# Kernel optimization log

Measured on AMD Instinct MI355X. Metric: run time of the kernel, lower is better.

## Reference

```python
import jax, jax.numpy as jnp
import numpy as np

B, P, N, C = 8, 4, 512, 768
H = 12
HD = C // H  # 64
SCALE = HD ** -0.5


def setup_inputs() -> dict:
    key = jax.random.key(0)
    k1, k2, k3 = jax.random.split(key, 3)
    x = jax.random.normal(k1, (B, P, N, C), dtype=jnp.float32)
    W_qkv = jax.random.normal(k2, (3 * C, C), dtype=jnp.float32) * (C ** -0.5)
    W_proj = jax.random.normal(k3, (C, C), dtype=jnp.float32) * (C ** -0.5)
    b_proj = jnp.zeros((C,), dtype=jnp.float32)
    return {"x": x, "W_qkv": W_qkv, "W_proj": W_proj, "b_proj": b_proj}


def reference(x, W_qkv, W_proj, b_proj):
    b, p, n, c = x.shape
    # qkv projection (no bias): (B,P,N,3C) -> (B,P,N,3,H,HD)
    qkv = jnp.einsum('bpnc,dc->bpnd', x, W_qkv).reshape(b, p, n, 3, H, HD)
    # -> (3, B, P, H, N, HD)
    qkv = jnp.transpose(qkv, (3, 0, 1, 4, 2, 5))
    q, k, v = qkv[0], qkv[1], qkv[2]
    # scaled dot-product attention per (batch, patch, head)
    attn = jnp.einsum('bphnd,bphmd->bphnm', q * SCALE, k)
    attn = jax.nn.softmax(attn, axis=-1)
    out = jnp.einsum('bphnm,bphmd->bphnd', attn, v)
    # merge heads: (B,P,N,H,HD) -> (B,P,N,C)
    out = jnp.transpose(out, (0, 1, 3, 2, 4)).reshape(b, p, n, c)
    return jnp.einsum('bpnc,dc->bpnd', out, W_proj) + b_proj
```

## Files before the change

### kernel.cpp

```cpp
#include <hip/hip_runtime.h>

typedef _Float16 f16x8 __attribute__((ext_vector_type(8)));
typedef _Float16 f16x4 __attribute__((ext_vector_type(4)));
typedef unsigned short u16x8 __attribute__((ext_vector_type(8)));
typedef unsigned short u16x4 __attribute__((ext_vector_type(4)));
typedef float f32x4 __attribute__((ext_vector_type(4)));

#define GLOAD_LDS16(GP, LP)                                                        \
  __builtin_amdgcn_global_load_lds((const __attribute__((address_space(1))) void*)(GP), \
                                   (__attribute__((address_space(3))) void*)(LP), 16, 0, 0)

__device__ __forceinline__ unsigned int pkh(float a, float b) {
  return __builtin_bit_cast(unsigned int, __builtin_amdgcn_cvt_pkrtz(a, b));
}
__device__ __forceinline__ f16x8 ldfragh(const unsigned short* p) {
  return __builtin_bit_cast(f16x8, *(const u16x8*)p);
}
__device__ __forceinline__ f16x4 ldfragh4(const unsigned short* p) {
  return __builtin_bit_cast(f16x4, *(const u16x4*)p);
}
__device__ __forceinline__ f32x4 mfma32h(f16x8 a, f16x8 b, f32x4 c) {
  return __builtin_amdgcn_mfma_f32_16x16x32_f16(a, b, c, 0, 0, 0);
}
__device__ __forceinline__ f32x4 mfma16h(f16x4 a, f16x4 b, f32x4 c) {
  return __builtin_amdgcn_mfma_f32_16x16x16f16(a, b, c, 0, 0, 0);
}

#define MTOK   16384
#define CDIM   768
#define C3     2304
#define C2     1536
#define NX     12582912
#define NQW    1769472
#define NPW    589824

#define QSCALE_LOG2E 0.1803368801111204f

#define XB_OFF    0ul
#define WQKV_OFF  25165824ul
#define WPROJ_OFF 28704768ul
#define QK_OFF    29884416ul
#define VT_OFF    80216064ul

__global__ __launch_bounds__(256) void convert_kernel(
    const float* __restrict__ x, const float* __restrict__ wqkv,
    const float* __restrict__ wproj, unsigned short* __restrict__ xb,
    unsigned short* __restrict__ wqkvb, unsigned short* __restrict__ wprojb) {
  const int NX4 = NX / 4, NQ4 = NQW / 4, NP4 = NPW / 4;
  const int total = NX4 + NQ4 + NP4;
  for (int i = blockIdx.x * 256 + threadIdx.x; i < total; i += gridDim.x * 256) {
    const float4* src; unsigned short* dst; float scale = 1.f; int j;
    if (i < NX4) { src = (const float4*)x; dst = xb; j = i; }
    else if (i < NX4 + NQ4) {
      j = i - NX4; src = (const float4*)wqkv; dst = wqkvb;
      int d = (j * 4) / CDIM; if (d < CDIM) scale = QSCALE_LOG2E;
    } else { j = i - NX4 - NQ4; src = (const float4*)wproj; dst = wprojb; }
    float4 v = src[j];
    uint2 pk; pk.x = pkh(v.x * scale, v.y * scale); pk.y = pkh(v.z * scale, v.w * scale);
    *(uint2*)(dst + (long)j * 4) = pk;
  }
}

template <int MODE, int NTN>
__global__ __launch_bounds__(512, 2) void gemm256(
    const unsigned short* __restrict__ A, const unsigned short* __restrict__ B,
    unsigned short* __restrict__ out_hf, unsigned short* __restrict__ out_vT,
    float* __restrict__ out_f32, const float* __restrict__ bias) {
  constexpr int K = 768;
  constexpr int NKT = K / 32;
  __shared__ unsigned short As[4][256 * 32];
  __shared__ unsigned short Bs[4][256 * 32];
  const int tid = threadIdx.x;
  const int wave = tid >> 6, lane = tid & 63;
  const int wy = wave >> 2, wx = wave & 3;
  const int l15 = lane & 15, quad = lane >> 4;

  const int gid = blockIdx.x;
  const int bn = (gid >> 3) % NTN;
  const int bm = ((gid >> 3) / NTN) * 8 + (gid & 7);
  const bool swap = (MODE == 2) || (bn < 6);

  f32x4 acc[8][4];
#pragma unroll
  for (int i = 0; i < 8; i++)
#pragma unroll
    for (int j = 0; j < 4; j++) acc[i][j] = f32x4{0.f, 0.f, 0.f, 0.f};

  const unsigned short* Ab = A + (long)bm * 256 * K;
  const unsigned short* Bb = B + (long)bn * 256 * K;

  const int c0 = wave * 128 + lane;
  const int c1 = c0 + 64;
  const int r0 = c0 >> 2, r1 = c1 >> 2;
  const long g0 = (long)r0 * K + (long)(((c0 & 3) ^ ((r0 >> 2) & 3)) * 8);
  const long g1 = (long)r1 * K + (long)(((c1 & 3) ^ ((r1 >> 2) & 3)) * 8);
  const int s0 = c0 * 8, s1 = c1 * 8;

#define STAGE_A(kt) { GLOAD_LDS16(Ab + g0 + (kt) * 32, &As[(kt) & 3][s0]); \
                      GLOAD_LDS16(Ab + g1 + (kt) * 32, &As[(kt) & 3][s1]); }
#define STAGE_B(kt) { GLOAD_LDS16(Bb + g0 + (kt) * 32, &Bs[(kt) & 3][s0]); \
                      GLOAD_LDS16(Bb + g1 + (kt) * 32, &Bs[(kt) & 3][s1]); }

  STAGE_A(0); STAGE_B(0); STAGE_A(1); STAGE_B(1); STAGE_A(2); STAGE_B(2);
  asm volatile("s_waitcnt vmcnt(8)" ::: "memory");
  __builtin_amdgcn_s_barrier();

  const int pho = (quad ^ (l15 >> 2)) * 8;
  const int arow = wy * 128 + l15;
  const int brow = wx * 64 + l15;

  for (int kt = 0; kt < NKT; kt++) {
    const unsigned short* Ac = As[kt & 3];
    const unsigned short* Bc = Bs[kt & 3];
    f16x8 af[4], bf[4];
#pragma unroll
    for (int nt = 0; nt < 4; nt++) bf[nt] = ldfragh(Bc + (brow + nt * 16) * 32 + pho);
#pragma unroll
    for (int mt = 0; mt < 4; mt++) af[mt] = ldfragh(Ac + (arow + mt * 16) * 32 + pho);
    if (kt < NKT - 3) STAGE_A(kt + 3);
    __builtin_amdgcn_s_barrier();
    asm volatile("s_waitcnt lgkmcnt(0)" ::: "memory");
    __builtin_amdgcn_s_setprio(1);
    if (swap) {
#pragma unroll
      for (int mt = 0; mt < 4; mt++)
#pragma unroll
        for (int nt = 0; nt < 4; nt++)
          acc[mt][nt] = mfma32h(bf[nt], af[mt], acc[mt][nt]);
    } else {
#pragma unroll
      for (int mt = 0; mt < 4; mt++)
#pragma unroll
        for (int nt = 0; nt < 4; nt++)
          acc[mt][nt] = mfma32h(af[mt], bf[nt], acc[mt][nt]);
    }
    __builtin_amdgcn_s_setprio(0);
    __builtin_amdgcn_s_barrier();
#pragma unroll
    for (int mt = 0; mt < 4; mt++) af[mt] = ldfragh(Ac + (arow + 64 + mt * 16) * 32 + pho);
    if (kt < NKT - 3) STAGE_B(kt + 3);
    if (kt < NKT - 3)       { asm volatile("s_waitcnt vmcnt(8)" ::: "memory"); }
    else if (kt == NKT - 3) { asm volatile("s_waitcnt vmcnt(4)" ::: "memory"); }
    else if (kt == NKT - 2) { asm volatile("s_waitcnt vmcnt(0)" ::: "memory"); }
    __builtin_amdgcn_s_barrier();
    asm volatile("s_waitcnt lgkmcnt(0)" ::: "memory");
    __builtin_amdgcn_s_setprio(1);
    if (swap) {
#pragma unroll
      for (int mt = 0; mt < 4; mt++)
#pragma unroll
        for (int nt = 0; nt < 4; nt++)
          acc[4 + mt][nt] = mfma32h(bf[nt], af[mt], acc[4 + mt][nt]);
    } else {
#pragma unroll
      for (int mt = 0; mt < 4; mt++)
#pragma unroll
        for (int nt = 0; nt < 4; nt++)
          acc[4 + mt][nt] = mfma32h(af[mt], bf[nt], acc[4 + mt][nt]);
    }
    __builtin_amdgcn_s_setprio(0);
    __builtin_amdgcn_s_barrier();
  }
#undef STAGE_A
#undef STAGE_B

  if (MODE == 0) {
    if (swap) {
#pragma unroll
      for (int mt = 0; mt < 8; mt++) {
        int m = bm * 256 + wy * 128 + mt * 16 + l15;
#pragma unroll
        for (int nt = 0; nt < 4; nt++) {
          int d0 = bn * 256 + wx * 64 + nt * 16 + quad * 4;
          uint2 pk; pk.x = pkh(acc[mt][nt][0], acc[mt][nt][1]);
          pk.y = pkh(acc[mt][nt][2], acc[mt][nt][3]);
          *(uint2*)(out_hf + (long)m * C2 + d0) = pk;
        }
      }
    } else {
#pragma unroll
      for (int mt = 0; mt < 8; mt++) {
        int mg = bm * 256 + wy * 128 + mt * 16 + quad * 4;
        int bp = mg >> 9, n0 = mg & 511;
#pragma unroll
        for (int nt = 0; nt < 4; nt++) {
          int dp = (bn - 6) * 256 + wx * 64 + nt * 16 + l15;
          int hh = dp >> 6, e = dp & 63;
          uint2 pk; pk.x = pkh(acc[mt][nt][0], acc[mt][nt][1]);
          pk.y = pkh(acc[mt][nt][2], acc[mt][nt][3]);
          *(uint2*)(out_vT + ((long)((bp * 12 + hh) * 64 + e) * 512 + n0)) = pk;
        }
      }
    }
  } else {
#pragma unroll
    for (int nt = 0; nt < 4; nt++) {
      int d0 = bn * 256 + wx * 64 + nt * 16 + quad * 4;
      float4 bv = *(const float4*)(bias + d0);
#pragma unroll
      for (int mt = 0; mt < 8; mt++) {
        int m = bm * 256 + wy * 128 + mt * 16 + l15;
        float4 o;
        o.x = acc[mt][nt][0] + bv.x; o.y = acc[mt][nt][1] + bv.y;
        o.z = acc[mt][nt][2] + bv.z; o.w = acc[mt][nt][3] + bv.w;
        *(float4*)(out_f32 + (long)m * CDIM + d0) = o;
      }
    }
  }
}

__global__ __launch_bounds__(256, 4) void attn_kernel(
    const unsigned short* __restrict__ qk, const unsigned short* __restrict__ vT,
    unsigned short* __restrict__ aout) {
  const int bph = blockIdx.x;
  const int qt  = blockIdx.y;
  const int bp = bph / 12, h = bph % 12;
  const int tid = threadIdx.x;
  const int wave = tid >> 6, lane = tid & 63;
  const int l15 = lane & 15, quad = lane >> 4;

  __shared__ unsigned short Qs[128 * 72];
  __shared__ unsigned short Ks[64 * 72];
  __shared__ unsigned short Vs[64 * 72];

  const unsigned short* Qg = qk + (long)(bp * 512 + qt * 128) * C2 + h * 64;
  const unsigned short* Kg = qk + (long)(bp * 512) * C2 + CDIM + h * 64;
  const unsigned short* Vg = vT + (long)(bp * 12 + h) * 64 * 512;

  for (int i = 0; i < 4; i++) {
    int c = tid + i * 256;
    int row = c >> 3, c8 = c & 7;
    *(uint4*)(Qs + row * 72 + c8 * 8) = *(const uint4*)(Qg + (long)row * C2 + c8 * 8);
  }

  f32x4 o[2][4];
  float lrow[2] = {0.f, 0.f};
  for (int a = 0; a < 2; a++)
    for (int b = 0; b < 4; b++) o[a][b] = f32x4{0.f, 0.f, 0.f, 0.f};

  for (int ch = 0; ch < 8; ch++) {
    if (ch) __syncthreads();
    for (int i = 0; i < 2; i++) {
      int c = tid + i * 256;
      int row = c >> 3, c8 = c & 7;
      *(uint4*)(Ks + row * 72 + c8 * 8) = *(const uint4*)(Kg + (long)(ch * 64 + row) * C2 + c8 * 8);
      *(uint4*)(Vs + row * 72 + c8 * 8) = *(const uint4*)(Vg + (long)row * 512 + ch * 64 + c8 * 8);
    }
    __syncthreads();

    f32x4 st[2][4];
    for (int a = 0; a < 2; a++)
      for (int b = 0; b < 4; b++) st[a][b] = f32x4{0.f, 0.f, 0.f, 0.f};
    for (int ks = 0; ks < 2; ks++) {
      f16x8 qf[2];
      qf[0] = ldfragh(Qs + (wave * 32 +      l15) * 72 + ks * 32 + quad * 8);
      qf[1] = ldfragh(Qs + (wave * 32 + 16 + l15) * 72 + ks * 32 + quad * 8);
      for (int nt = 0; nt < 4; nt++) {
        f16x8 kf = ldfragh(Ks + (nt * 16 + l15) * 72 + ks * 32 + quad * 8);
        st[0][nt] = mfma32h(kf, qf[0], st[0][nt]);
        st[1][nt] = mfma32h(kf, qf[1], st[1][nt]);
      }
    }

    f16x4 pf[2][4];
    for (int mt2 = 0; mt2 < 2; mt2++) {
      float rs = 0.f;
      for (int nt = 0; nt < 4; nt++) {
        f32x4 p;
        for (int r = 0; r < 4; r++) {
          p[r] = __builtin_amdgcn_exp2f(st[mt2][nt][r]);
          rs += p[r];
        }
        uint2 pk2; pk2.x = pkh(p[0], p[1]); pk2.y = pkh(p[2], p[3]);
        pf[mt2][nt] = __builtin_bit_cast(f16x4, pk2);
      }
      lrow[mt2] += rs;
    }

    for (int nt = 0; nt < 4; nt++)
      for (int et = 0; et < 4; et++) {
        f16x4 vf = ldfragh4(Vs + (et * 16 + l15) * 72 + nt * 16 + quad * 4);
        o[0][et] = mfma16h(vf, pf[0][nt], o[0][et]);
        o[1][et] = mfma16h(vf, pf[1][nt], o[1][et]);
      }
  }

  for (int mt2 = 0; mt2 < 2; mt2++) {
    float l = lrow[mt2];
    l += __shfl_xor(l, 16);
    l += __shfl_xor(l, 32);
    float inv = 1.f / l;
    int q = qt * 128 + wave * 32 + mt2 * 16 + l15;
    for (int et = 0; et < 4; et++) {
      uint2 pk; pk.x = pkh(o[mt2][et][0] * inv, o[mt2][et][1] * inv);
      pk.y = pkh(o[mt2][et][2] * inv, o[mt2][et][3] * inv);
      *(uint2*)(aout + (long)(bp * 512 + q) * CDIM + h * 64 + et * 16 + quad * 4) = pk;
    }
  }
}

extern "C" void kernel_launch(void* const* d_in, const int* in_sizes, int n_in,
                              void* d_out, int out_size, void* d_ws, size_t ws_size,
                              hipStream_t stream) {
  (void)in_sizes; (void)n_in; (void)out_size; (void)ws_size;
  const float* x     = (const float*)d_in[0];
  const float* wqkv  = (const float*)d_in[1];
  const float* wproj = (const float*)d_in[2];
  const float* bproj = (const float*)d_in[3];
  float* out = (float*)d_out;
  char* ws = (char*)d_ws;

  unsigned short* xb     = (unsigned short*)(ws + XB_OFF);
  unsigned short* wqkvb  = (unsigned short*)(ws + WQKV_OFF);
  unsigned short* wprojb = (unsigned short*)(ws + WPROJ_OFF);
  unsigned short* qkbuf  = (unsigned short*)(ws + QK_OFF);
  unsigned short* vTbuf  = (unsigned short*)(ws + VT_OFF);
  unsigned short* attn_o = xb;

  convert_kernel<<<2048, 256, 0, stream>>>(x, wqkv, wproj, xb, wqkvb, wprojb);
  gemm256<0, 9><<<576, 512, 0, stream>>>(xb, wqkvb, qkbuf, vTbuf, nullptr, nullptr);
  attn_kernel<<<dim3(384, 4), 256, 0, stream>>>(qkbuf, vTbuf, attn_o);
  gemm256<2, 3><<<192, 512, 0, stream>>>(attn_o, wprojb, nullptr, nullptr, out, bproj);
}
```

Baseline: 290.3 us.

## Retile projection GEMMs to 256x192 tiles with new LDS layout and single barrier per k-step

Changes both GEMMs from 256x256 to 256x192 output tiles, raising the block count (768 and 256) so the 256-CU device gets fuller waves. It replaces the XOR-swizzled LDS staging with a paired-row interleaved layout and merges the two half-k-step phases into one loop body that loads all fragments, then issues 24 MFMAs behind a single barrier. Per-wave vmcnt waits differ because only half the threads stage the extra B chunk. The risks are LDS bank conflicts from the new layout, a WAR hazard on a 4-slot ring now guarded by a single barrier, and more fragment registers in flight.

```diff
diff --git a/kernel.cpp b/kernel.cpp
--- a/kernel.cpp
+++ b/kernel.cpp
@@ -62,14 +62,14 @@
 }
 
 template <int MODE, int NTN>
-__global__ __launch_bounds__(512, 2) void gemm256(
+__global__ __launch_bounds__(512, 2) void gemm192(
     const unsigned short* __restrict__ A, const unsigned short* __restrict__ B,
     unsigned short* __restrict__ out_hf, unsigned short* __restrict__ out_vT,
     float* __restrict__ out_f32, const float* __restrict__ bias) {
   constexpr int K = 768;
-  constexpr int NKT = K / 32;
-  __shared__ unsigned short As[4][256 * 32];
-  __shared__ unsigned short Bs[4][256 * 32];
+  constexpr int NKT = 24;
+  __shared__ unsigned short As[4][8192];
+  __shared__ unsigned short Bs[4][6144];
   const int tid = threadIdx.x;
   const int wave = tid >> 6, lane = tid & 63;
   const int wy = wave >> 2, wx = wave & 3;
@@ -78,91 +78,81 @@
   const int gid = blockIdx.x;
   const int bn = (gid >> 3) % NTN;
   const int bm = ((gid >> 3) / NTN) * 8 + (gid & 7);
-  const bool swap = (MODE == 2) || (bn < 6);
-
-  f32x4 acc[8][4];
+  const bool swap = (MODE == 2) || (bn < 8);
+
+  f32x4 acc[8][3];
 #pragma unroll
   for (int i = 0; i < 8; i++)
 #pragma unroll
-    for (int j = 0; j < 4; j++) acc[i][j] = f32x4{0.f, 0.f, 0.f, 0.f};
+    for (int j = 0; j < 3; j++) acc[i][j] = f32x4{0.f, 0.f, 0.f, 0.f};
 
   const unsigned short* Ab = A + (long)bm * 256 * K;
-  const unsigned short* Bb = B + (long)bn * 256 * K;
-
-  const int c0 = wave * 128 + lane;
-  const int c1 = c0 + 64;
-  const int r0 = c0 >> 2, r1 = c1 >> 2;
-  const long g0 = (long)r0 * K + (long)(((c0 & 3) ^ ((r0 >> 2) & 3)) * 8);
-  const long g1 = (long)r1 * K + (long)(((c1 & 3) ^ ((r1 >> 2) & 3)) * 8);
-  const int s0 = c0 * 8, s1 = c1 * 8;
-
-#define STAGE_A(kt) { GLOAD_LDS16(Ab + g0 + (kt) * 32, &As[(kt) & 3][s0]); \
-                      GLOAD_LDS16(Ab + g1 + (kt) * 32, &As[(kt) & 3][s1]); }
-#define STAGE_B(kt) { GLOAD_LDS16(Bb + g0 + (kt) * 32, &Bs[(kt) & 3][s0]); \
-                      GLOAD_LDS16(Bb + g1 + (kt) * 32, &Bs[(kt) & 3][s1]); }
-
-  STAGE_A(0); STAGE_B(0); STAGE_A(1); STAGE_B(1); STAGE_A(2); STAGE_B(2);
-  asm volatile("s_waitcnt vmcnt(8)" ::: "memory");
+  const unsigned short* Bb = B + (long)bn * 192 * K;
+
+  const int cA0 = tid, cA1 = tid + 512;
+  const int cB0 = tid, cB1 = tid + 512;
+  const bool extraB = (tid < 256);
+  const long gA0 = (long)(2 * (cA0 >> 3) + ((cA0 >> 2) & 1)) * K + (cA0 & 3) * 8;
+  const long gA1 = (long)(2 * (cA1 >> 3) + ((cA1 >> 2) & 1)) * K + (cA1 & 3) * 8;
+  const long gB0 = (long)(2 * (cB0 >> 3) + ((cB0 >> 2) & 1)) * K + (cB0 & 3) * 8;
+  const long gB1 = (long)(2 * (cB1 >> 3) + ((cB1 >> 2) & 1)) * K + (cB1 & 3) * 8;
+  const int sA0 = cA0 * 8, sA1 = cA1 * 8, sB0 = cB0 * 8, sB1 = cB1 * 8;
+
+#define STAGE(kt) { const long kk = (long)(kt) * 32; const int sl = (kt) & 3;      \
+    GLOAD_LDS16(Ab + gA0 + kk, &As[sl][sA0]);                                      \
+    GLOAD_LDS16(Ab + gA1 + kk, &As[sl][sA1]);                                      \
+    GLOAD_LDS16(Bb + gB0 + kk, &Bs[sl][sB0]);                                      \
+    if (extraB) GLOAD_LDS16(Bb + gB1 + kk, &Bs[sl][sB1]); }
+
+  STAGE(0); STAGE(1); STAGE(2);
+  if (wave < 4) { asm volatile("s_waitcnt vmcnt(8)" ::: "memory"); }
+  else          { asm volatile("s_waitcnt vmcnt(6)" ::: "memory"); }
   __builtin_amdgcn_s_barrier();
-
-  const int pho = (quad ^ (l15 >> 2)) * 8;
-  const int arow = wy * 128 + l15;
-  const int brow = wx * 64 + l15;
+  asm volatile("" ::: "memory");
+
+  const int rl = (l15 >> 1) * 64 + (l15 & 1) * 32 + quad * 8;
+  const int aoff = wy * 4096;
+  const int boff = wx * 1536;
 
   for (int kt = 0; kt < NKT; kt++) {
     const unsigned short* Ac = As[kt & 3];
     const unsigned short* Bc = Bs[kt & 3];
-    f16x8 af[4], bf[4];
-#pragma unroll
-    for (int nt = 0; nt < 4; nt++) bf[nt] = ldfragh(Bc + (brow + nt * 16) * 32 + pho);
-#pragma unroll
-    for (int mt = 0; mt < 4; mt++) af[mt] = ldfragh(Ac + (arow + mt * 16) * 32 + pho);
-    if (kt < NKT - 3) STAGE_A(kt + 3);
+    f16x8 af[8], bf[3];
+#pragma unroll
+    for (int mt = 0; mt < 8; mt++) af[mt] = ldfragh(Ac + aoff + mt * 512 + rl);
+#pragma unroll
+    for (int nt = 0; nt < 3; nt++) bf[nt] = ldfragh(Bc + boff + nt * 512 + rl);
+
+    if (kt < NKT - 3) {
+      STAGE(kt + 3);
+      if (wave < 4) { asm volatile("s_waitcnt vmcnt(8)" ::: "memory"); }
+      else          { asm volatile("s_waitcnt vmcnt(6)" ::: "memory"); }
+    } else if (kt == NKT - 3) {
+      if (wave < 4) { asm volatile("s_waitcnt vmcnt(4)" ::: "memory"); }
+      else          { asm volatile("s_waitcnt vmcnt(3)" ::: "memory"); }
+    } else if (kt == NKT - 2) {
+      asm volatile("s_waitcnt vmcnt(0)" ::: "memory");
+    }
     __builtin_amdgcn_s_barrier();
-    asm volatile("s_waitcnt lgkmcnt(0)" ::: "memory");
+    asm volatile("" ::: "memory");
+
     __builtin_amdgcn_s_setprio(1);
     if (swap) {
 #pragma unroll
-      for (int mt = 0; mt < 4; mt++)
-#pragma unroll
-        for (int nt = 0; nt < 4; nt++)
+      for (int mt = 0; mt < 8; mt++)
+#pragma unroll
+        for (int nt = 0; nt < 3; nt++)
           acc[mt][nt] = mfma32h(bf[nt], af[mt], acc[mt][nt]);
     } else {
 #pragma unroll
-      for (int mt = 0; mt < 4; mt++)
-#pragma unroll
-        for (int nt = 0; nt < 4; nt++)
+      for (int mt = 0; mt < 8; mt++)
+#pragma unroll
+        for (int nt = 0; nt < 3; nt++)
           acc[mt][nt] = mfma32h(af[mt], bf[nt], acc[mt][nt]);
     }
     __builtin_amdgcn_s_setprio(0);
-    __builtin_amdgcn_s_barrier();
-#pragma unroll
-    for (int mt = 0; mt < 4; mt++) af[mt] = ldfragh(Ac + (arow + 64 + mt * 16) * 32 + pho);
-    if (kt < NKT - 3) STAGE_B(kt + 3);
-    if (kt < NKT - 3)       { asm volatile("s_waitcnt vmcnt(8)" ::: "memory"); }
-    else if (kt == NKT - 3) { asm volatile("s_waitcnt vmcnt(4)" ::: "memory"); }
-    else if (kt == NKT - 2) { asm volatile("s_waitcnt vmcnt(0)" ::: "memory"); }
-    __builtin_amdgcn_s_barrier();
-    asm volatile("s_waitcnt lgkmcnt(0)" ::: "memory");
-    __builtin_amdgcn_s_setprio(1);
-    if (swap) {
-#pragma unroll
-      for (int mt = 0; mt < 4; mt++)
-#pragma unroll
-        for (int nt = 0; nt < 4; nt++)
-          acc[4 + mt][nt] = mfma32h(bf[nt], af[mt], acc[4 + mt][nt]);
-    } else {
-#pragma unroll
-      for (int mt = 0; mt < 4; mt++)
-#pragma unroll
-        for (int nt = 0; nt < 4; nt++)
-          acc[4 + mt][nt] = mfma32h(af[mt], bf[nt], acc[4 + mt][nt]);
-    }
-    __builtin_amdgcn_s_setprio(0);
-    __builtin_amdgcn_s_barrier();
-  }
-#undef STAGE_A
-#undef STAGE_B
+  }
+#undef STAGE
 
   if (MODE == 0) {
     if (swap) {
@@ -170,8 +160,8 @@
       for (int mt = 0; mt < 8; mt++) {
         int m = bm * 256 + wy * 128 + mt * 16 + l15;
 #pragma unroll
-        for (int nt = 0; nt < 4; nt++) {
-          int d0 = bn * 256 + wx * 64 + nt * 16 + quad * 4;
+        for (int nt = 0; nt < 3; nt++) {
+          int d0 = bn * 192 + wx * 48 + nt * 16 + quad * 4;
           uint2 pk; pk.x = pkh(acc[mt][nt][0], acc[mt][nt][1]);
           pk.y = pkh(acc[mt][nt][2], acc[mt][nt][3]);
           *(uint2*)(out_hf + (long)m * C2 + d0) = pk;
@@ -183,8 +173,8 @@
         int mg = bm * 256 + wy * 128 + mt * 16 + quad * 4;
         int bp = mg >> 9, n0 = mg & 511;
 #pragma unroll
-        for (int nt = 0; nt < 4; nt++) {
-          int dp = (bn - 6) * 256 + wx * 64 + nt * 16 + l15;
+        for (int nt = 0; nt < 3; nt++) {
+          int dp = (bn - 8) * 192 + wx * 48 + nt * 16 + l15;
           int hh = dp >> 6, e = dp & 63;
           uint2 pk; pk.x = pkh(acc[mt][nt][0], acc[mt][nt][1]);
           pk.y = pkh(acc[mt][nt][2], acc[mt][nt][3]);
@@ -194,8 +184,8 @@
     }
   } else {
 #pragma unroll
-    for (int nt = 0; nt < 4; nt++) {
-      int d0 = bn * 256 + wx * 64 + nt * 16 + quad * 4;
+    for (int nt = 0; nt < 3; nt++) {
+      int d0 = bn * 192 + wx * 48 + nt * 16 + quad * 4;
       float4 bv = *(const float4*)(bias + d0);
 #pragma unroll
       for (int mt = 0; mt < 8; mt++) {
@@ -318,7 +308,7 @@
   unsigned short* attn_o = xb;
 
   convert_kernel<<<2048, 256, 0, stream>>>(x, wqkv, wproj, xb, wqkvb, wprojb);
-  gemm256<0, 9><<<576, 512, 0, stream>>>(xb, wqkvb, qkbuf, vTbuf, nullptr, nullptr);
+  gemm192<0, 12><<<768, 512, 0, stream>>>(xb, wqkvb, qkbuf, vTbuf, nullptr, nullptr);
   attn_kernel<<<dim3(384, 4), 256, 0, stream>>>(qkbuf, vTbuf, attn_o);
-  gemm256<2, 3><<<192, 512, 0, stream>>>(attn_o, wprojb, nullptr, nullptr, out, bproj);
-}
+  gemm192<2, 4><<<256, 512, 0, stream>>>(attn_o, wprojb, nullptr, nullptr, out, bproj);
+}
```

Result: faster. 272.6 us (-6.1%).

## Restructure GEMM mainloop to 64-wide K tiles with quadrant-split staging

Applied to the files above, without the earlier changes.

Rewrites the 256x256 GEMM mainloop to use K=64 tiles (12 iterations instead of 24), stored as two 128-row halves per operand with double buffering. Each iteration runs in four MFMA phases, and the loads for each half-tile are interleaved between phases with explicit vmcnt waits, barriers and sched_barrier fences. Wave-to-output mapping changes so each wave covers interleaved 64-row/32-col sub-blocks, and the epilogue index math is updated to match. The goal is to cut barrier and loop overhead per FLOP and overlap global-to-LDS traffic with MFMA more finely, at the cost of a more fragile hand-tuned wait schedule and a changed LDS swizzle.

```diff
diff --git a/kernel.cpp b/kernel.cpp
--- a/kernel.cpp
+++ b/kernel.cpp
@@ -67,17 +67,18 @@
     unsigned short* __restrict__ out_hf, unsigned short* __restrict__ out_vT,
     float* __restrict__ out_f32, const float* __restrict__ bias) {
   constexpr int K = 768;
-  constexpr int NKT = K / 32;
-  __shared__ unsigned short As[4][256 * 32];
-  __shared__ unsigned short Bs[4][256 * 32];
+  constexpr int NKT = 12;
+  __shared__ unsigned short As[2][2][128 * 64];
+  __shared__ unsigned short Bs[2][2][128 * 64];
   const int tid = threadIdx.x;
   const int wave = tid >> 6, lane = tid & 63;
   const int wy = wave >> 2, wx = wave & 3;
   const int l15 = lane & 15, quad = lane >> 4;
 
   const int gid = blockIdx.x;
-  const int bn = (gid >> 3) % NTN;
-  const int bm = ((gid >> 3) / NTN) * 8 + (gid & 7);
+  const int g = gid >> 3;
+  const int bn = g % NTN;
+  const int bm = (g / NTN) * 8 + (gid & 7);
   const bool swap = (MODE == 2) || (bn < 6);
 
   f32x4 acc[8][4];
@@ -89,120 +90,146 @@
   const unsigned short* Ab = A + (long)bm * 256 * K;
   const unsigned short* Bb = B + (long)bn * 256 * K;
 
-  const int c0 = wave * 128 + lane;
-  const int c1 = c0 + 64;
-  const int r0 = c0 >> 2, r1 = c1 >> 2;
-  const long g0 = (long)r0 * K + (long)(((c0 & 3) ^ ((r0 >> 2) & 3)) * 8);
-  const long g1 = (long)r1 * K + (long)(((c1 & 3) ^ ((r1 >> 2) & 3)) * 8);
+  const int c0 = tid, c1 = tid + 512;
+  const long gof0 = (long)(c0 >> 3) * K + (long)(((c0 & 7) ^ ((c0 >> 3) & 7)) * 8);
+  const long gof1 = (long)(c1 >> 3) * K + (long)(((c1 & 7) ^ ((c1 >> 3) & 7)) * 8);
   const int s0 = c0 * 8, s1 = c1 * 8;
 
-#define STAGE_A(kt) { GLOAD_LDS16(Ab + g0 + (kt) * 32, &As[(kt) & 3][s0]); \
-                      GLOAD_LDS16(Ab + g1 + (kt) * 32, &As[(kt) & 3][s1]); }
-#define STAGE_B(kt) { GLOAD_LDS16(Bb + g0 + (kt) * 32, &Bs[(kt) & 3][s0]); \
-                      GLOAD_LDS16(Bb + g1 + (kt) * 32, &Bs[(kt) & 3][s1]); }
-
-  STAGE_A(0); STAGE_B(0); STAGE_A(1); STAGE_B(1); STAGE_A(2); STAGE_B(2);
-  asm volatile("s_waitcnt vmcnt(8)" ::: "memory");
-  __builtin_amdgcn_s_barrier();
-
-  const int pho = (quad ^ (l15 >> 2)) * 8;
-  const int arow = wy * 128 + l15;
-  const int brow = wx * 64 + l15;
-
-  for (int kt = 0; kt < NKT; kt++) {
-    const unsigned short* Ac = As[kt & 3];
-    const unsigned short* Bc = Bs[kt & 3];
-    f16x8 af[4], bf[4];
-#pragma unroll
-    for (int nt = 0; nt < 4; nt++) bf[nt] = ldfragh(Bc + (brow + nt * 16) * 32 + pho);
-#pragma unroll
-    for (int mt = 0; mt < 4; mt++) af[mt] = ldfragh(Ac + (arow + mt * 16) * 32 + pho);
-    if (kt < NKT - 3) STAGE_A(kt + 3);
-    __builtin_amdgcn_s_barrier();
-    asm volatile("s_waitcnt lgkmcnt(0)" ::: "memory");
-    __builtin_amdgcn_s_setprio(1);
-    if (swap) {
-#pragma unroll
-      for (int mt = 0; mt < 4; mt++)
-#pragma unroll
-        for (int nt = 0; nt < 4; nt++)
-          acc[mt][nt] = mfma32h(bf[nt], af[mt], acc[mt][nt]);
-    } else {
-#pragma unroll
-      for (int mt = 0; mt < 4; mt++)
-#pragma unroll
-        for (int nt = 0; nt < 4; nt++)
-          acc[mt][nt] = mfma32h(af[mt], bf[nt], acc[mt][nt]);
-    }
-    __builtin_amdgcn_s_setprio(0);
-    __builtin_amdgcn_s_barrier();
-#pragma unroll
-    for (int mt = 0; mt < 4; mt++) af[mt] = ldfragh(Ac + (arow + 64 + mt * 16) * 32 + pho);
-    if (kt < NKT - 3) STAGE_B(kt + 3);
-    if (kt < NKT - 3)       { asm volatile("s_waitcnt vmcnt(8)" ::: "memory"); }
-    else if (kt == NKT - 3) { asm volatile("s_waitcnt vmcnt(4)" ::: "memory"); }
-    else if (kt == NKT - 2) { asm volatile("s_waitcnt vmcnt(0)" ::: "memory"); }
-    __builtin_amdgcn_s_barrier();
-    asm volatile("s_waitcnt lgkmcnt(0)" ::: "memory");
-    __builtin_amdgcn_s_setprio(1);
-    if (swap) {
-#pragma unroll
-      for (int mt = 0; mt < 4; mt++)
-#pragma unroll
-        for (int nt = 0; nt < 4; nt++)
-          acc[4 + mt][nt] = mfma32h(bf[nt], af[mt], acc[4 + mt][nt]);
-    } else {
-#pragma unroll
-      for (int mt = 0; mt < 4; mt++)
-#pragma unroll
-        for (int nt = 0; nt < 4; nt++)
-          acc[4 + mt][nt] = mfma32h(af[mt], bf[nt], acc[4 + mt][nt]);
-    }
-    __builtin_amdgcn_s_setprio(0);
-    __builtin_amdgcn_s_barrier();
-  }
-#undef STAGE_A
-#undef STAGE_B
+#define STAGE(DST, GBASE, kt) {                                   \
+    const unsigned short* gsrc_ = (GBASE) + (long)(kt) * 64;      \
+    GLOAD_LDS16(gsrc_ + gof0, &(DST)[s0]);                        \
+    GLOAD_LDS16(gsrc_ + gof1, &(DST)[s1]); }
+#define A0G (Ab)
+#define A1G (Ab + 128 * K)
+#define B0G (Bb)
+#define B1G (Bb + 128 * K)
+#define BAR() { asm volatile("" ::: "memory"); __builtin_amdgcn_s_barrier(); \
+                asm volatile("" ::: "memory"); }
+#define SCHED0() __builtin_amdgcn_sched_barrier(0)
+#define LGKM0() { asm volatile("s_waitcnt lgkmcnt(0)" ::: "memory"); SCHED0(); }
+#define VMW(N)  { asm volatile("s_waitcnt vmcnt(" #N ")" ::: "memory"); SCHED0(); }
+
+  STAGE(As[0][0], A0G, 0); STAGE(Bs[0][0], B0G, 0); STAGE(Bs[0][1], B1G, 0);
+  STAGE(As[0][1], A1G, 0); STAGE(As[1][0], A0G, 1); STAGE(Bs[1][0], B0G, 1);
+  VMW(6);
+  BAR();
+
+  const int sl0 = ((quad)     ^ (l15 & 7)) * 8;
+  const int sl1 = ((4 + quad) ^ (l15 & 7)) * 8;
+  const int ar = (wy * 64 + l15) * 64;
+  const int br = ((wx & 1) * 64 + l15) * 64;
+
+#define MFMA_PHASE(MH, NH)                                                   \
+  __builtin_amdgcn_s_setprio(1);                                             \
+  if (swap) {                                                                \
+    _Pragma("unroll") for (int m = 0; m < 4; m++)                            \
+      _Pragma("unroll") for (int n = 0; n < 2; n++)                          \
+        _Pragma("unroll") for (int ks = 0; ks < 2; ks++)                     \
+          acc[(MH)*4 + m][(NH)*2 + n] =                                      \
+            mfma32h(bf[NH][n][ks], af[m][ks], acc[(MH)*4 + m][(NH)*2 + n]);  \
+  } else {                                                                   \
+    _Pragma("unroll") for (int m = 0; m < 4; m++)                            \
+      _Pragma("unroll") for (int n = 0; n < 2; n++)                          \
+        _Pragma("unroll") for (int ks = 0; ks < 2; ks++)                     \
+          acc[(MH)*4 + m][(NH)*2 + n] =                                      \
+            mfma32h(af[m][ks], bf[NH][n][ks], acc[(MH)*4 + m][(NH)*2 + n]);  \
+  }                                                                          \
+  __builtin_amdgcn_s_setprio(0)
+
+#pragma unroll 2
+  for (int t = 0; t < NKT; t++) {
+    const unsigned short* Ac0 = &As[t & 1][0][0];
+    const unsigned short* Ac1 = &As[t & 1][1][0];
+    const unsigned short* Bcw = &Bs[t & 1][wx >> 1][0];
+    const int nb = (t + 1) & 1;
+    f16x8 af[4][2], bf[2][2][2];
+
+#pragma unroll
+    for (int m = 0; m < 4; m++) {
+      af[m][0] = ldfragh(Ac0 + ar + m * 1024 + sl0);
+      af[m][1] = ldfragh(Ac0 + ar + m * 1024 + sl1);
+    }
+#pragma unroll
+    for (int n = 0; n < 2; n++) {
+      bf[0][n][0] = ldfragh(Bcw + br + n * 1024 + sl0);
+      bf[0][n][1] = ldfragh(Bcw + br + n * 1024 + sl1);
+    }
+    if (t <= 10) STAGE(Bs[nb][1], B1G, t + 1);
+    BAR(); LGKM0();
+    MFMA_PHASE(0, 0);
+    BAR();
+
+#pragma unroll
+    for (int n = 0; n < 2; n++) {
+      bf[1][n][0] = ldfragh(Bcw + br + (2 + n) * 1024 + sl0);
+      bf[1][n][1] = ldfragh(Bcw + br + (2 + n) * 1024 + sl1);
+    }
+    if (t <= 10) STAGE(As[nb][1], A1G, t + 1);
+    if (t <= 10) { VMW(8); }
+    else         { VMW(0); }
+    BAR(); LGKM0();
+    MFMA_PHASE(0, 1);
+    BAR();
+
+#pragma unroll
+    for (int m = 0; m < 4; m++) {
+      af[m][0] = ldfragh(Ac1 + ar + m * 1024 + sl0);
+      af[m][1] = ldfragh(Ac1 + ar + m * 1024 + sl1);
+    }
+    if (t <= 9) STAGE(As[t & 1][0], A0G, t + 2);
+    BAR(); LGKM0();
+    MFMA_PHASE(1, 0);
+    BAR();
+
+    if (t <= 9) STAGE(Bs[t & 1][0], B0G, t + 2);
+    if (t <= 9)       { VMW(6); }
+    else if (t == 10) { VMW(2); }
+    BAR();
+    MFMA_PHASE(1, 1);
+    BAR();
+  }
+#undef STAGE
+#undef MFMA_PHASE
 
   if (MODE == 0) {
     if (swap) {
 #pragma unroll
-      for (int mt = 0; mt < 8; mt++) {
-        int m = bm * 256 + wy * 128 + mt * 16 + l15;
-#pragma unroll
-        for (int nt = 0; nt < 4; nt++) {
-          int d0 = bn * 256 + wx * 64 + nt * 16 + quad * 4;
-          uint2 pk; pk.x = pkh(acc[mt][nt][0], acc[mt][nt][1]);
-          pk.y = pkh(acc[mt][nt][2], acc[mt][nt][3]);
+      for (int mi = 0; mi < 8; mi++) {
+        int m = bm * 256 + (mi >> 2) * 128 + wy * 64 + (mi & 3) * 16 + l15;
+#pragma unroll
+        for (int ni = 0; ni < 4; ni++) {
+          int d0 = bn * 256 + wx * 64 + (ni >> 1) * 32 + (ni & 1) * 16 + quad * 4;
+          uint2 pk; pk.x = pkh(acc[mi][ni][0], acc[mi][ni][1]);
+          pk.y = pkh(acc[mi][ni][2], acc[mi][ni][3]);
           *(uint2*)(out_hf + (long)m * C2 + d0) = pk;
         }
       }
     } else {
 #pragma unroll
-      for (int mt = 0; mt < 8; mt++) {
-        int mg = bm * 256 + wy * 128 + mt * 16 + quad * 4;
+      for (int mi = 0; mi < 8; mi++) {
+        int mg = bm * 256 + (mi >> 2) * 128 + wy * 64 + (mi & 3) * 16 + quad * 4;
         int bp = mg >> 9, n0 = mg & 511;
 #pragma unroll
-        for (int nt = 0; nt < 4; nt++) {
-          int dp = (bn - 6) * 256 + wx * 64 + nt * 16 + l15;
+        for (int ni = 0; ni < 4; ni++) {
+          int dp = (bn - 6) * 256 + wx * 64 + (ni >> 1) * 32 + (ni & 1) * 16 + l15;
           int hh = dp >> 6, e = dp & 63;
-          uint2 pk; pk.x = pkh(acc[mt][nt][0], acc[mt][nt][1]);
-          pk.y = pkh(acc[mt][nt][2], acc[mt][nt][3]);
+          uint2 pk; pk.x = pkh(acc[mi][ni][0], acc[mi][ni][1]);
+          pk.y = pkh(acc[mi][ni][2], acc[mi][ni][3]);
           *(uint2*)(out_vT + ((long)((bp * 12 + hh) * 64 + e) * 512 + n0)) = pk;
         }
       }
     }
   } else {
 #pragma unroll
-    for (int nt = 0; nt < 4; nt++) {
-      int d0 = bn * 256 + wx * 64 + nt * 16 + quad * 4;
+    for (int ni = 0; ni < 4; ni++) {
+      int d0 = bn * 256 + wx * 64 + (ni >> 1) * 32 + (ni & 1) * 16 + quad * 4;
       float4 bv = *(const float4*)(bias + d0);
 #pragma unroll
-      for (int mt = 0; mt < 8; mt++) {
-        int m = bm * 256 + wy * 128 + mt * 16 + l15;
+      for (int mi = 0; mi < 8; mi++) {
+        int m = bm * 256 + (mi >> 2) * 128 + wy * 64 + (mi & 3) * 16 + l15;
         float4 o;
-        o.x = acc[mt][nt][0] + bv.x; o.y = acc[mt][nt][1] + bv.y;
-        o.z = acc[mt][nt][2] + bv.z; o.w = acc[mt][nt][3] + bv.w;
+        o.x = acc[mi][ni][0] + bv.x; o.y = acc[mi][ni][1] + bv.y;
+        o.z = acc[mi][ni][2] + bv.z; o.w = acc[mi][ni][3] + bv.w;
         *(float4*)(out_f32 + (long)m * CDIM + d0) = o;
       }
     }
```

After: 350.2 us. 20.6% more time.
